# Kernel tuning notes

Measured on AMD Instinct MI355X. Metric: run time of the kernel, lower is better.

The kernel has to match this reference:

```python
import jax, jax.numpy as jnp
import numpy as np

IGNORE_INDEX = -100


def setup_inputs() -> dict:
    key = jax.random.key(0)
    k1, k2, k3 = jax.random.split(key, 3)
    VOCAB, D = 32000, 2048
    B, S = 4, 2048
    weight = jax.random.normal(k1, (VOCAB, D), dtype=jnp.float32) * 0.02
    hidden = jax.random.normal(k2, (B, S, D), dtype=jnp.float32)
    targets = jax.random.randint(k3, (B, S), 0, VOCAB, dtype=jnp.int64)
    return {"weight": weight, "hidden": hidden, "targets": targets}


def reference(weight, hidden, targets):
    # Fused linear + cross-entropy: loss = sum_t CE(hidden_t @ W^T, target_t) / n_valid.
    # (The torch module chunks over sequence purely to save memory; the math is
    # identical to the unchunked computation below.)
    B, S, D = hidden.shape
    flat_h = hidden.reshape(-1, D)            # [B*S, D]
    flat_t = targets.reshape(-1)              # [B*S]
    logits = (flat_h @ weight.T).astype(jnp.float32)  # [B*S, V]
    lse = jax.nn.logsumexp(logits, axis=-1)   # [B*S]
    safe_t = jnp.clip(flat_t, 0, logits.shape[-1] - 1)
    tgt_logit = jnp.take_along_axis(logits, safe_t[:, None], axis=-1)[:, 0]
    valid = flat_t != IGNORE_INDEX
    per_tok = jnp.where(valid, lse - tgt_logit, 0.0)
    total_loss = per_tok.sum()
    n_valid = valid.sum().astype(jnp.float32)
    return jnp.where(n_valid > 0, total_loss / n_valid, total_loss)
```

## Files before the change

### kernel.cpp

```cpp
#include <hip/hip_runtime.h>

#define IGNORE_INDEX (-100)
#define VOCAB 32000
#define DDIM  2048
#define MTOK  8192

#define BM 256
#define BN 128
#define BK 128
#define NKT (DDIM / BK)

#define WSCALE 32.0f
#define HSCALE 8.0f
#define INVSCALE (1.0f / 256.0f)
#define SCALE_ONE 0x7F7F7F7F

#define WBLK ((VOCAB * DDIM) / (256 * 16))
#define HBLK ((MTOK * DDIM) / (256 * 16))
#define ZBLK ((2 * MTOK * 4) / (256 * 16))

typedef float f32x4 __attribute__((ext_vector_type(4)));
typedef int   i32x8 __attribute__((ext_vector_type(8)));
typedef unsigned char uchar_t;

__device__ __forceinline__ void cvt16(const float4* __restrict__ src,
                                      int4* __restrict__ dst, float scale,
                                      size_t i) {
    float4 a = src[4 * i], b = src[4 * i + 1], c = src[4 * i + 2], d = src[4 * i + 3];
    int4 o;
    int v;
    v = 0;
    v = __builtin_amdgcn_cvt_pk_fp8_f32(a.x * scale, a.y * scale, v, false);
    v = __builtin_amdgcn_cvt_pk_fp8_f32(a.z * scale, a.w * scale, v, true);
    o.x = v;
    v = 0;
    v = __builtin_amdgcn_cvt_pk_fp8_f32(b.x * scale, b.y * scale, v, false);
    v = __builtin_amdgcn_cvt_pk_fp8_f32(b.z * scale, b.w * scale, v, true);
    o.y = v;
    v = 0;
    v = __builtin_amdgcn_cvt_pk_fp8_f32(c.x * scale, c.y * scale, v, false);
    v = __builtin_amdgcn_cvt_pk_fp8_f32(c.z * scale, c.w * scale, v, true);
    o.z = v;
    v = 0;
    v = __builtin_amdgcn_cvt_pk_fp8_f32(d.x * scale, d.y * scale, v, false);
    v = __builtin_amdgcn_cvt_pk_fp8_f32(d.z * scale, d.w * scale, v, true);
    o.w = v;
    dst[i] = o;
}

__global__ void cvt_f32_fp8(const float4* __restrict__ srcW, int4* __restrict__ dstW,
                            const float4* __restrict__ srcH, int4* __restrict__ dstH,
                            int4* __restrict__ zr) {
    if (blockIdx.x < WBLK) {
        size_t i = (size_t)blockIdx.x * blockDim.x + threadIdx.x;
        cvt16(srcW, dstW, WSCALE, i);
    } else if (blockIdx.x < WBLK + HBLK) {
        size_t i = (size_t)(blockIdx.x - WBLK) * blockDim.x + threadIdx.x;
        cvt16(srcH, dstH, HSCALE, i);
    } else {
        int i = (blockIdx.x - WBLK - HBLK) * 256 + threadIdx.x;
        zr[i] = make_int4(0, 0, 0, 0);
    }
}

__device__ __forceinline__ void load_lds16(const uchar_t* g, uchar_t* l) {
    __builtin_amdgcn_global_load_lds(
        (const __attribute__((address_space(1))) unsigned int*)(const void*)g,
        (__attribute__((address_space(3))) unsigned int*)(void*)l,
        16, 0, 0);
}

__device__ __forceinline__ i32x8 read_frag(const uchar_t* arr, int off) {
    int4 lo = *reinterpret_cast<const int4*>(arr + off);
    int4 hi = *reinterpret_cast<const int4*>(arr + (off ^ 16));
    i32x8 r;
    r[0] = lo.x; r[1] = lo.y; r[2] = lo.z; r[3] = lo.w;
    r[4] = hi.x; r[5] = hi.y; r[6] = hi.z; r[7] = hi.w;
    return r;
}

__global__ __launch_bounds__(512, 2) void gemm_ce(
    const uchar_t* __restrict__ A,
    const uchar_t* __restrict__ B,
    const int* __restrict__ targets,
    float* __restrict__ sumexp,
    float* __restrict__ tgtlogit) {
    __shared__ alignas(16) uchar_t As[3][BM * BK];
    __shared__ alignas(16) uchar_t Bs[3][BN * BK];

    const int tid  = threadIdx.x;
    const int wave = tid >> 6;
    const int lane = tid & 63;
    const int quad = lane >> 4;
    const int l16  = lane & 15;
    const int wm   = (wave >> 1) * 64;
    const int wn   = (wave & 1) * 64;

    const int m0 = blockIdx.x * BM;
    const int n0 = blockIdx.y * BN;

    const int srow = lane >> 3;
    const int sswz = ((lane & 7) ^ srow) << 4;
    const uchar_t* Ag = A + (size_t)(m0 + wave * 32 + srow) * DDIM + sswz;
    const uchar_t* Bg = B + (size_t)(n0 + wave * 16 + srow) * DDIM + sswz;

    const int swlo = ((quad << 1) ^ (l16 & 7)) << 4;
    const int aoff = (wm + l16) * BK + swlo;
    const int boff = (wn + l16) * BK + swlo;

    f32x4 acc[4][4];
    const f32x4 zero = {0.f, 0.f, 0.f, 0.f};
#pragma unroll
    for (int i = 0; i < 4; ++i)
#pragma unroll
        for (int j = 0; j < 4; ++j) acc[i][j] = zero;

#define STAGE(buf, kk)                                                         \
    do {                                                                       \
        uchar_t* a_ = &As[0][0] + (buf) * (BM * BK) + (wave * 32) * BK;        \
        uchar_t* b_ = &Bs[0][0] + (buf) * (BN * BK) + (wave * 16) * BK;        \
        _Pragma("unroll") for (int it_ = 0; it_ < 4; ++it_)                    \
            load_lds16(Ag + (size_t)it_ * 8 * DDIM + (kk), a_ + it_ * 8 * BK); \
        _Pragma("unroll") for (int it_ = 0; it_ < 2; ++it_)                    \
            load_lds16(Bg + (size_t)it_ * 8 * DDIM + (kk), b_ + it_ * 8 * BK); \
    } while (0)

#define COMPUTE(buf)                                                           \
    do {                                                                       \
        const uchar_t* as_ = &As[0][0] + (buf) * (BM * BK);                    \
        const uchar_t* bs_ = &Bs[0][0] + (buf) * (BN * BK);                    \
        i32x8 af[4], bf[4];                                                    \
        _Pragma("unroll") for (int i_ = 0; i_ < 4; ++i_)                       \
            af[i_] = read_frag(as_, aoff + i_ * 16 * BK);                      \
        _Pragma("unroll") for (int j_ = 0; j_ < 4; ++j_)                       \
            bf[j_] = read_frag(bs_, boff + j_ * 16 * BK);                      \
        PREFETCH;                                                              \
        __builtin_amdgcn_s_setprio(1);                                         \
        _Pragma("unroll") for (int i_ = 0; i_ < 4; ++i_)                       \
            _Pragma("unroll") for (int j_ = 0; j_ < 4; ++j_)                   \
                acc[i_][j_] = __builtin_amdgcn_mfma_scale_f32_16x16x128_f8f6f4(\
                    af[i_], bf[j_], acc[i_][j_],                               \
                    0, 0, 0, SCALE_ONE, 0, SCALE_ONE);                         \
        __builtin_amdgcn_s_setprio(0);                                         \
    } while (0)

#define VMCNT(n) asm volatile("s_waitcnt vmcnt(" #n ")" ::: "memory")
#define BARRIER  asm volatile("s_barrier" ::: "memory")

    STAGE(0, 0);
    STAGE(1, BK);

    int cur = 0, stg = 2;
#pragma clang loop unroll(disable)
    for (int t = 0; t < NKT - 2; ++t) {
        VMCNT(6);
        BARRIER;
#define PREFETCH STAGE(stg, (t + 2) * BK)
        COMPUTE(cur);
#undef PREFETCH
        cur = (cur == 2) ? 0 : cur + 1;
        stg = (stg == 2) ? 0 : stg + 1;
    }
#define PREFETCH
    VMCNT(6);
    BARRIER;
    COMPUTE(cur);
    cur = (cur == 2) ? 0 : cur + 1;
    VMCNT(0);
    BARRIER;
    COMPUTE(cur);
#undef PREFETCH

    __syncthreads();
    float* sred = reinterpret_cast<float*>(&As[0][0]);
#pragma unroll
    for (int i = 0; i < 4; ++i) {
#pragma unroll
        for (int r = 0; r < 4; ++r) {
            const int rloc = wm + i * 16 + quad * 4 + r;
            const int mg = m0 + rloc;
            const int t  = targets[mg];
            float p = 0.f;
#pragma unroll
            for (int j = 0; j < 4; ++j) {
                float v = acc[i][j][r] * INVSCALE;
                p += __expf(v);
                if (t == n0 + wn + j * 16 + l16) tgtlogit[mg] = v;
            }
            p += __shfl_xor(p, 1);
            p += __shfl_xor(p, 2);
            p += __shfl_xor(p, 4);
            p += __shfl_xor(p, 8);
            if (l16 == 0) sred[(wave & 1) * 256 + rloc] = p;
        }
    }
    __syncthreads();
    if (tid < 256) {
        float s = sred[tid] + sred[256 + tid];
        atomicAdd(&sumexp[m0 + tid], s);
    }

#undef STAGE
#undef COMPUTE
#undef VMCNT
#undef BARRIER
}

__global__ void finalize(const float* __restrict__ sumexp,
                         const float* __restrict__ tgtlogit,
                         const int* __restrict__ targets,
                         float* __restrict__ out) {
    __shared__ float s_sum[16];
    __shared__ float s_cnt[16];
    float local = 0.f, cnt = 0.f;
    for (int t = threadIdx.x; t < MTOK; t += blockDim.x) {
        int tg = targets[t];
        if (tg != IGNORE_INDEX) {
            local += logf(sumexp[t]) - tgtlogit[t];
            cnt += 1.f;
        }
    }
#pragma unroll
    for (int o = 32; o > 0; o >>= 1) {
        local += __shfl_down(local, o);
        cnt   += __shfl_down(cnt, o);
    }
    const int wave = threadIdx.x >> 6, lane = threadIdx.x & 63;
    if (lane == 0) { s_sum[wave] = local; s_cnt[wave] = cnt; }
    __syncthreads();
    if (threadIdx.x == 0) {
        float ts = 0.f, tc = 0.f;
        for (int w = 0; w < (int)(blockDim.x >> 6); ++w) {
            ts += s_sum[w];
            tc += s_cnt[w];
        }
        out[0] = (tc > 0.f) ? (ts / tc) : ts;
    }
}

extern "C" void kernel_launch(void* const* d_in, const int* in_sizes, int n_in,
                              void* d_out, int out_size, void* d_ws,
                              size_t ws_size, hipStream_t stream) {
    const float* weight  = (const float*)d_in[0];
    const float* hidden  = (const float*)d_in[1];
    const int*   targets = (const int*)d_in[2];
    float* out = (float*)d_out;

    const size_t wbytes = (size_t)VOCAB * DDIM;
    const size_t hbytes = (size_t)MTOK * DDIM;
    uchar_t* Wb = (uchar_t*)d_ws;
    uchar_t* Hb = (uchar_t*)d_ws + wbytes;
    float* sumexp   = (float*)((char*)d_ws + wbytes + hbytes);
    float* tgtlogit = sumexp + MTOK;

    cvt_f32_fp8<<<WBLK + HBLK + ZBLK, 256, 0, stream>>>(
        (const float4*)weight, (int4*)Wb, (const float4*)hidden, (int4*)Hb,
        (int4*)sumexp);

    dim3 grid(MTOK / BM, VOCAB / BN);
    gemm_ce<<<grid, 512, 0, stream>>>(Hb, Wb, targets, sumexp, tgtlogit);

    finalize<<<1, 1024, 0, stream>>>(sumexp, tgtlogit, targets, out);
}
```

Baseline: 988.9 us.

## Widen GEMM tile to 256x256 with double-buffered LDS pipeline

Doubles the N dimension of the block tile so each wave computes a 128x64 sub-tile with twice the accumulators. This raises arithmetic intensity per LDS byte and halves the number of column blocks that re-read the hidden activations. To fit in LDS, the three-stage prefetch ring becomes a two-stage double buffer with a full vmcnt(0) wait each iteration. The row-sum reduction is widened to four column waves. The risks are register pressure from 128 accumulator floats under the unchanged launch bounds, and less latency hiding from the shallower pipeline.

```diff
diff --git a/kernel.cpp b/kernel.cpp
--- a/kernel.cpp
+++ b/kernel.cpp
@@ -6,7 +6,7 @@
 #define MTOK  8192
 
 #define BM 256
-#define BN 128
+#define BN 256
 #define BK 128
 #define NKT (DDIM / BK)
 
@@ -85,16 +85,16 @@
     const int* __restrict__ targets,
     float* __restrict__ sumexp,
     float* __restrict__ tgtlogit) {
-    __shared__ alignas(16) uchar_t As[3][BM * BK];
-    __shared__ alignas(16) uchar_t Bs[3][BN * BK];
+    __shared__ alignas(16) uchar_t As[2][BM * BK];
+    __shared__ alignas(16) uchar_t Bs[2][BN * BK];
 
     const int tid  = threadIdx.x;
     const int wave = tid >> 6;
     const int lane = tid & 63;
     const int quad = lane >> 4;
     const int l16  = lane & 15;
-    const int wm   = (wave >> 1) * 64;
-    const int wn   = (wave & 1) * 64;
+    const int wm   = (wave >> 2) * 128;
+    const int wn   = (wave & 3) * 64;
 
     const int m0 = blockIdx.x * BM;
     const int n0 = blockIdx.y * BN;
@@ -102,79 +102,82 @@
     const int srow = lane >> 3;
     const int sswz = ((lane & 7) ^ srow) << 4;
     const uchar_t* Ag = A + (size_t)(m0 + wave * 32 + srow) * DDIM + sswz;
-    const uchar_t* Bg = B + (size_t)(n0 + wave * 16 + srow) * DDIM + sswz;
+    const uchar_t* Bg = B + (size_t)(n0 + wave * 32 + srow) * DDIM + sswz;
 
     const int swlo = ((quad << 1) ^ (l16 & 7)) << 4;
     const int aoff = (wm + l16) * BK + swlo;
     const int boff = (wn + l16) * BK + swlo;
 
-    f32x4 acc[4][4];
+    f32x4 acc[8][4];
     const f32x4 zero = {0.f, 0.f, 0.f, 0.f};
 #pragma unroll
-    for (int i = 0; i < 4; ++i)
+    for (int i = 0; i < 8; ++i)
 #pragma unroll
         for (int j = 0; j < 4; ++j) acc[i][j] = zero;
 
 #define STAGE(buf, kk)                                                         \
     do {                                                                       \
-        uchar_t* a_ = &As[0][0] + (buf) * (BM * BK) + (wave * 32) * BK;        \
-        uchar_t* b_ = &Bs[0][0] + (buf) * (BN * BK) + (wave * 16) * BK;        \
+        uchar_t* a_ = &As[buf][0] + (wave * 32) * BK;                          \
+        uchar_t* b_ = &Bs[buf][0] + (wave * 32) * BK;                          \
         _Pragma("unroll") for (int it_ = 0; it_ < 4; ++it_)                    \
             load_lds16(Ag + (size_t)it_ * 8 * DDIM + (kk), a_ + it_ * 8 * BK); \
-        _Pragma("unroll") for (int it_ = 0; it_ < 2; ++it_)                    \
+        _Pragma("unroll") for (int it_ = 0; it_ < 4; ++it_)                    \
             load_lds16(Bg + (size_t)it_ * 8 * DDIM + (kk), b_ + it_ * 8 * BK); \
     } while (0)
 
 #define COMPUTE(buf)                                                           \
     do {                                                                       \
-        const uchar_t* as_ = &As[0][0] + (buf) * (BM * BK);                    \
-        const uchar_t* bs_ = &Bs[0][0] + (buf) * (BN * BK);                    \
-        i32x8 af[4], bf[4];                                                    \
-        _Pragma("unroll") for (int i_ = 0; i_ < 4; ++i_)                       \
-            af[i_] = read_frag(as_, aoff + i_ * 16 * BK);                      \
+        const uchar_t* as_ = &As[buf][0];                                      \
+        const uchar_t* bs_ = &Bs[buf][0];                                      \
+        i32x8 bfr[4], afA[4];                                                  \
         _Pragma("unroll") for (int j_ = 0; j_ < 4; ++j_)                       \
-            bf[j_] = read_frag(bs_, boff + j_ * 16 * BK);                      \
+            bfr[j_] = read_frag(bs_, boff + j_ * 16 * BK);                     \
+        _Pragma("unroll") for (int i_ = 0; i_ < 4; ++i_)                       \
+            afA[i_] = read_frag(as_, aoff + i_ * 16 * BK);                     \
         PREFETCH;                                                              \
         __builtin_amdgcn_s_setprio(1);                                         \
         _Pragma("unroll") for (int i_ = 0; i_ < 4; ++i_)                       \
             _Pragma("unroll") for (int j_ = 0; j_ < 4; ++j_)                   \
                 acc[i_][j_] = __builtin_amdgcn_mfma_scale_f32_16x16x128_f8f6f4(\
-                    af[i_], bf[j_], acc[i_][j_],                               \
+                    afA[i_], bfr[j_], acc[i_][j_],                             \
+                    0, 0, 0, SCALE_ONE, 0, SCALE_ONE);                         \
+        __builtin_amdgcn_s_setprio(0);                                         \
+        i32x8 afB[4];                                                          \
+        _Pragma("unroll") for (int i_ = 0; i_ < 4; ++i_)                       \
+            afB[i_] = read_frag(as_, aoff + (i_ + 4) * 16 * BK);               \
+        __builtin_amdgcn_s_setprio(1);                                         \
+        _Pragma("unroll") for (int i_ = 0; i_ < 4; ++i_)                       \
+            _Pragma("unroll") for (int j_ = 0; j_ < 4; ++j_)                   \
+                acc[i_ + 4][j_] = __builtin_amdgcn_mfma_scale_f32_16x16x128_f8f6f4(\
+                    afB[i_], bfr[j_], acc[i_ + 4][j_],                         \
                     0, 0, 0, SCALE_ONE, 0, SCALE_ONE);                         \
         __builtin_amdgcn_s_setprio(0);                                         \
     } while (0)
 
-#define VMCNT(n) asm volatile("s_waitcnt vmcnt(" #n ")" ::: "memory")
-#define BARRIER  asm volatile("s_barrier" ::: "memory")
+#define VMCNT0  asm volatile("s_waitcnt vmcnt(0)" ::: "memory")
+#define BARRIER asm volatile("s_barrier" ::: "memory")
 
     STAGE(0, 0);
-    STAGE(1, BK);
-
-    int cur = 0, stg = 2;
+    VMCNT0;
+    BARRIER;
+
 #pragma clang loop unroll(disable)
-    for (int t = 0; t < NKT - 2; ++t) {
-        VMCNT(6);
-        BARRIER;
-#define PREFETCH STAGE(stg, (t + 2) * BK)
+    for (int t = 0; t < NKT - 1; ++t) {
+        const int cur = t & 1;
+#define PREFETCH STAGE(cur ^ 1, (t + 1) * BK)
         COMPUTE(cur);
 #undef PREFETCH
-        cur = (cur == 2) ? 0 : cur + 1;
-        stg = (stg == 2) ? 0 : stg + 1;
+        VMCNT0;
+        BARRIER;
     }
 #define PREFETCH
-    VMCNT(6);
-    BARRIER;
-    COMPUTE(cur);
-    cur = (cur == 2) ? 0 : cur + 1;
-    VMCNT(0);
-    BARRIER;
-    COMPUTE(cur);
+    COMPUTE(1);
 #undef PREFETCH
 
     __syncthreads();
     float* sred = reinterpret_cast<float*>(&As[0][0]);
 #pragma unroll
-    for (int i = 0; i < 4; ++i) {
+    for (int i = 0; i < 8; ++i) {
 #pragma unroll
         for (int r = 0; r < 4; ++r) {
             const int rloc = wm + i * 16 + quad * 4 + r;
@@ -191,18 +194,18 @@
             p += __shfl_xor(p, 2);
             p += __shfl_xor(p, 4);
             p += __shfl_xor(p, 8);
-            if (l16 == 0) sred[(wave & 1) * 256 + rloc] = p;
+            if (l16 == 0) sred[(wave & 3) * 256 + rloc] = p;
         }
     }
     __syncthreads();
     if (tid < 256) {
-        float s = sred[tid] + sred[256 + tid];
+        float s = sred[tid] + sred[256 + tid] + sred[512 + tid] + sred[768 + tid];
         atomicAdd(&sumexp[m0 + tid], s);
     }
 
 #undef STAGE
 #undef COMPUTE
-#undef VMCNT
+#undef VMCNT0
 #undef BARRIER
 }
 
```

Measured after the change: 934.9 us. 1.06x faster.
